# Kernel optimization log

Hardware: AMD Instinct MI355X
Metric: run time of the kernel (lower is better)

Reference implementation:

```python
import jax, jax.numpy as jnp
import numpy as np

B, T, DIM = 8, 2048, 512
DM, EXPAND, NSTATE, HDIM, L = 128, 2, 16, 64, 2
DINNER = DM * EXPAND            # 256
NH = DINNER // HDIM             # 4 heads
CONVDIM = DINNER + 2 * NSTATE   # 288 (n_groups=1)
PROJ = DINNER + CONVDIM + NH    # 548
K = 4                           # conv kernel (HF default)
EPS = 1e-5


def setup_inputs() -> dict:
    key = jax.random.key(0)
    ks = jax.random.split(key, 8)
    s = 0.02
    return {
        "x": jax.random.normal(ks[0], (B, T, DIM), jnp.float32),
        "in_w": jax.random.normal(ks[1], (DIM, DM), jnp.float32) * s,
        "in_b": jnp.zeros((DM,), jnp.float32),
        "norm_w": jnp.ones((L, DM), jnp.float32),
        "inproj_w": jax.random.normal(ks[2], (L, DM, PROJ), jnp.float32) * s,
        "conv_w": jax.random.normal(ks[3], (L, CONVDIM, 1, K), jnp.float32) * 0.2,
        "conv_b": jnp.zeros((L, CONVDIM), jnp.float32),
        "A_log": jnp.log(jax.random.uniform(ks[4], (L, NH), jnp.float32, 1.0, 8.0)),
        "D": jnp.ones((L, NH), jnp.float32),
        "dt_bias": jnp.log(jnp.expm1(jax.random.uniform(ks[5], (L, NH), jnp.float32, 1e-3, 0.1))),
        "gnorm_w": jnp.ones((L, DINNER), jnp.float32),
        "outproj_w": jax.random.normal(ks[6], (L, DINNER, DM), jnp.float32) * s,
        "normf_w": jnp.ones((DM,), jnp.float32),
        "out_w": jax.random.normal(ks[7], (DM, DIM), jnp.float32) * s,
        "out_b": jnp.zeros((DIM,), jnp.float32),
    }


def _rmsnorm(x, w):
    var = jnp.mean(x * x, axis=-1, keepdims=True)
    return x * jax.lax.rsqrt(var + EPS) * w


def _gated_rmsnorm(y, gate, w):
    y = y * jax.nn.silu(gate)
    var = jnp.mean(y * y, axis=-1, keepdims=True)
    return y * jax.lax.rsqrt(var + EPS) * w


def _causal_conv(h, w, b):
    # h: [B,T,C] depthwise causal conv, kernel K, left pad K-1
    out = jax.lax.conv_general_dilated(
        h.swapaxes(1, 2), w, (1,), [(K - 1, 0)],
        feature_group_count=CONVDIM,
        dimension_numbers=("NCH", "OIH", "NCH"))
    return out.swapaxes(1, 2) + b


def _ssd(xs, dt, A, Bm, Cm, Dh):
    # selective state-space scan (math-equivalent to HF Mamba2 chunked SSD)
    # xs [B,T,H,P], dt [B,T,H], A [H], Bm/Cm [B,T,N], Dh [H]
    dA = jnp.exp(dt * A)  # [B,T,H]

    def step(state, inp):
        dA_t, dt_t, x_t, B_t, C_t = inp
        dBx = dt_t[:, :, None, None] * x_t[..., None] * B_t[:, None, None, :]
        state = state * dA_t[:, :, None, None] + dBx  # [B,H,P,N]
        y = jnp.einsum("bhpn,bn->bhp", state, C_t)
        return state, y

    init = jnp.zeros((xs.shape[0], NH, HDIM, NSTATE), xs.dtype)
    _, ys = jax.lax.scan(step, init, (dA.swapaxes(0, 1), dt.swapaxes(0, 1),
                                      xs.swapaxes(0, 1), Bm.swapaxes(0, 1), Cm.swapaxes(0, 1)))
    return ys.swapaxes(0, 1) + xs * Dh[None, None, :, None]


def reference(x, in_w, in_b, norm_w, inproj_w, conv_w, conv_b, A_log, D,
              dt_bias, gnorm_w, outproj_w, normf_w, out_w, out_b):
    h = x @ in_w + in_b  # [B,T,DM]
    for l in range(L):
        res = h
        hn = _rmsnorm(h, norm_w[l])
        proj = hn @ inproj_w[l]  # [B,T,PROJ]
        gate = proj[..., :DINNER]
        hBC = proj[..., DINNER:DINNER + CONVDIM]
        dt = proj[..., DINNER + CONVDIM:]
        hBC = jax.nn.silu(_causal_conv(hBC, conv_w[l], conv_b[l]))
        xs = hBC[..., :DINNER].reshape(B, T, NH, HDIM)
        Bm = hBC[..., DINNER:DINNER + NSTATE]
        Cm = hBC[..., DINNER + NSTATE:]
        A = -jnp.exp(A_log[l])
        dt = jax.nn.softplus(dt + dt_bias[l])  # time_step_limit=(0,inf): no clamp
        y = _ssd(xs, dt, A, Bm, Cm, D[l]).reshape(B, T, DINNER)
        y = _gated_rmsnorm(y, gate, gnorm_w[l])
        h = res + y @ outproj_w[l]
    h = _rmsnorm(h, normf_w)
    pooled = h.mean(axis=1)  # mean pool over T
    return pooled @ out_w + out_b
```

## Files before the change

kernel.cpp:

```cpp
#include <hip/hip_runtime.h>
#include <math.h>

typedef unsigned short ushort_t;
typedef unsigned int uint_t;

#define B_      8
#define T_      2048
#define DIMX    512
#define DM      128
#define DINNER  256
#define NSTATE  16
#define HDIM    64
#define NH      4
#define CONVDIM 288
#define PROJ    548
#define KCONV   4
#define LLAYERS 2
#define QCH     128
#define NC      (T_/QCH)
#define EPSF    1e-5f
#define MTOK    (B_*T_)

#define OFF_H      0u
#define OFF_Z      20119552u
#define OFF_DEC    21168128u
#define OFF_PART   21168640u
#define OFF_WTIN   23396864u
#define OFF_WTINP  23429632u
#define OFF_WTOUT  23503360u
#define OFF_PROJB  23600000u
#define OFF_DTRAW  28100000u
#define OFF_YB     30600000u

__device__ __forceinline__ ushort_t f2b(float f) {
    uint_t u = __builtin_bit_cast(uint_t, f);
    return (ushort_t)((u + 0x7FFFu + ((u >> 16) & 1u)) >> 16);
}
__device__ __forceinline__ float b2f(ushort_t b) {
    uint_t u = ((uint_t)b) << 16;
    return __builtin_bit_cast(float, u);
}
__device__ __forceinline__ float blo(uint_t u) { return b2f((ushort_t)(u & 0xffffu)); }
__device__ __forceinline__ float bhi(uint_t u) { return b2f((ushort_t)(u >> 16)); }

typedef short bf8 __attribute__((ext_vector_type(8)));
typedef float f4v __attribute__((ext_vector_type(4)));

__global__ __launch_bounds__(256) void k_wt_all(
    const float* __restrict__ in_w, const float* __restrict__ inproj_w,
    const float* __restrict__ outproj_w,
    ushort_t* __restrict__ wt_in, ushort_t* __restrict__ wt_inp,
    ushort_t* __restrict__ wt_out)
{
    __shared__ float tile[64][65];
    int idx = blockIdx.x;
    const float* W; ushort_t* Wt; int K, N, k0, n0;
    if (idx < 16) {
        W = in_w; Wt = wt_in; K = 512; N = 128;
        k0 = (idx & 7) * 64; n0 = (idx >> 3) * 64;
    } else if (idx < 52) {
        int r = idx - 16; int l = r / 18; r -= l * 18;
        W = inproj_w + l * 128 * PROJ; Wt = wt_inp + l * 576 * 128; K = 128; N = PROJ;
        k0 = (r & 1) * 64; n0 = (r >> 1) * 64;
    } else {
        int r = idx - 52; int l = r / 8; r -= l * 8;
        W = outproj_w + l * 256 * 128; Wt = wt_out + l * 128 * 256; K = 256; N = 128;
        k0 = (r & 3) * 64; n0 = (r >> 2) * 64;
    }
    const int tid = threadIdx.x;
#pragma unroll
    for (int it = 0; it < 16; ++it) {
        const int e = it * 256 + tid;
        const int kk = e >> 6, nn = e & 63;
        tile[kk][nn] = (n0 + nn < N) ? W[(k0 + kk) * N + (n0 + nn)] : 0.f;
    }
    __syncthreads();
#pragma unroll
    for (int it = 0; it < 16; ++it) {
        const int e = it * 256 + tid;
        const int nn = e >> 6, kk = e & 63;
        Wt[(n0 + nn) * K + k0 + kk] = f2b(tile[kk][nn]);
    }
}

__global__ __launch_bounds__(256) void k_gemm_in(
    const float* __restrict__ x, const ushort_t* __restrict__ Bt,
    const float* __restrict__ ib, float* __restrict__ C)
{
    __shared__ ushort_t Als[64 * 136];
    __shared__ ushort_t Bls[64 * 136];
    const int m0 = blockIdx.x * 64;
    const int tid = threadIdx.x;
    const int lane = tid & 63, w = tid >> 6;
    const int wm = (w >> 1) * 32, wn = (w & 1) * 32;
    const int r16 = lane & 15, q8 = (lane >> 4) * 8;

    f4v acc[2][2][2];
#pragma unroll
    for (int hf = 0; hf < 2; ++hf)
#pragma unroll
        for (int i = 0; i < 2; ++i)
#pragma unroll
            for (int j = 0; j < 2; ++j) acc[hf][i][j] = (f4v)0.f;

    for (int kc = 0; kc < 512; kc += 128) {
#pragma unroll
        for (int i = 0; i < 4; ++i) {
            const int e = i * 2048 + tid * 8;
            const int r = e >> 7, c = e & 127;
            const float4 f0 = *(const float4*)&x[(m0 + r) * 512 + kc + c];
            const float4 f1 = *(const float4*)&x[(m0 + r) * 512 + kc + c + 4];
            uint4 pk;
            pk.x = (uint_t)f2b(f0.x) | ((uint_t)f2b(f0.y) << 16);
            pk.y = (uint_t)f2b(f0.z) | ((uint_t)f2b(f0.w) << 16);
            pk.z = (uint_t)f2b(f1.x) | ((uint_t)f2b(f1.y) << 16);
            pk.w = (uint_t)f2b(f1.z) | ((uint_t)f2b(f1.w) << 16);
            *(uint4*)&Als[r * 136 + c] = pk;
        }
#pragma unroll
        for (int hf = 0; hf < 2; ++hf) {
            const int n0 = hf * 64;
#pragma unroll
            for (int i = 0; i < 4; ++i) {
                const int e = i * 2048 + tid * 8;
                const int r = e >> 7, c = e & 127;
                *(uint4*)&Bls[r * 136 + c] = *(const uint4*)&Bt[(n0 + r) * 512 + kc + c];
            }
            __syncthreads();
#pragma unroll
            for (int kk = 0; kk < 128; kk += 32) {
                const bf8 a0 = *(const bf8*)&Als[(wm + r16) * 136 + kk + q8];
                const bf8 a1 = *(const bf8*)&Als[(wm + 16 + r16) * 136 + kk + q8];
                const bf8 b0 = *(const bf8*)&Bls[(wn + r16) * 136 + kk + q8];
                const bf8 b1 = *(const bf8*)&Bls[(wn + 16 + r16) * 136 + kk + q8];
                acc[hf][0][0] = __builtin_amdgcn_mfma_f32_16x16x32_bf16(a0, b0, acc[hf][0][0], 0, 0, 0);
                acc[hf][0][1] = __builtin_amdgcn_mfma_f32_16x16x32_bf16(a0, b1, acc[hf][0][1], 0, 0, 0);
                acc[hf][1][0] = __builtin_amdgcn_mfma_f32_16x16x32_bf16(a1, b0, acc[hf][1][0], 0, 0, 0);
                acc[hf][1][1] = __builtin_amdgcn_mfma_f32_16x16x32_bf16(a1, b1, acc[hf][1][1], 0, 0, 0);
            }
            __syncthreads();
        }
    }
    const int q4 = (lane >> 4) * 4;
#pragma unroll
    for (int hf = 0; hf < 2; ++hf)
#pragma unroll
        for (int i = 0; i < 2; ++i)
#pragma unroll
            for (int j = 0; j < 2; ++j)
#pragma unroll
                for (int r = 0; r < 4; ++r) {
                    const int grow = m0 + wm + i * 16 + q4 + r;
                    const int gcol = hf * 64 + wn + j * 16 + r16;
                    C[grow * 128 + gcol] = acc[hf][i][j][r] + ib[gcol];
                }
}

__global__ __launch_bounds__(256) void k_gemm_rms(
    const float* __restrict__ h, const float* __restrict__ nw,
    const ushort_t* __restrict__ Bt, ushort_t* __restrict__ projb,
    float* __restrict__ dtraw)
{
    __shared__ ushort_t Als[64 * 136];
    __shared__ ushort_t Bls[64 * 136];
    const int m0 = blockIdx.x * 64;
    const int tid = threadIdx.x;
    const int lane = tid & 63, w = tid >> 6;
    const int wm = (w >> 1) * 32, wn = (w & 1) * 32;
    const int r16 = lane & 15, q8 = (lane >> 4) * 8;
    const int q4 = (lane >> 4) * 4;

#pragma unroll
    for (int i = 0; i < 4; ++i) {
        const int e = i * 2048 + tid * 8;
        const int r = e >> 7, c = e & 127;
        const float4 f0 = *(const float4*)&h[(m0 + r) * 128 + c];
        const float4 f1 = *(const float4*)&h[(m0 + r) * 128 + c + 4];
        float ss = f0.x * f0.x + f0.y * f0.y + f0.z * f0.z + f0.w * f0.w
                 + f1.x * f1.x + f1.y * f1.y + f1.z * f1.z + f1.w * f1.w;
#pragma unroll
        for (int off = 1; off < 16; off <<= 1) ss += __shfl_xor(ss, off);
        const float rs = rsqrtf(ss * (1.f / 128.f) + EPSF);
        const float4 w0 = *(const float4*)&nw[c];
        const float4 w1 = *(const float4*)&nw[c + 4];
        uint4 pk;
        pk.x = (uint_t)f2b(f0.x * rs * w0.x) | ((uint_t)f2b(f0.y * rs * w0.y) << 16);
        pk.y = (uint_t)f2b(f0.z * rs * w0.z) | ((uint_t)f2b(f0.w * rs * w0.w) << 16);
        pk.z = (uint_t)f2b(f1.x * rs * w1.x) | ((uint_t)f2b(f1.y * rs * w1.y) << 16);
        pk.w = (uint_t)f2b(f1.z * rs * w1.z) | ((uint_t)f2b(f1.w * rs * w1.w) << 16);
        *(uint4*)&Als[r * 136 + c] = pk;
    }

#pragma unroll
    for (int half = 0; half < 2; ++half) {
        const int n0 = blockIdx.y * 128 + half * 64;
        if (n0 >= 576) break;
#pragma unroll
        for (int i = 0; i < 4; ++i) {
            const int e = i * 2048 + tid * 8;
            const int r = e >> 7, c = e & 127;
            *(uint4*)&Bls[r * 136 + c] = *(const uint4*)&Bt[(n0 + r) * 128 + c];
        }
        __syncthreads();

        f4v acc[2][2];
#pragma unroll
        for (int i = 0; i < 2; ++i)
#pragma unroll
            for (int j = 0; j < 2; ++j) acc[i][j] = (f4v)0.f;
#pragma unroll
        for (int kk = 0; kk < 128; kk += 32) {
            const bf8 a0 = *(const bf8*)&Als[(wm + r16) * 136 + kk + q8];
            const bf8 a1 = *(const bf8*)&Als[(wm + 16 + r16) * 136 + kk + q8];
            const bf8 b0 = *(const bf8*)&Bls[(wn + r16) * 136 + kk + q8];
            const bf8 b1 = *(const bf8*)&Bls[(wn + 16 + r16) * 136 + kk + q8];
            acc[0][0] = __builtin_amdgcn_mfma_f32_16x16x32_bf16(a0, b0, acc[0][0], 0, 0, 0);
            acc[0][1] = __builtin_amdgcn_mfma_f32_16x16x32_bf16(a0, b1, acc[0][1], 0, 0, 0);
            acc[1][0] = __builtin_amdgcn_mfma_f32_16x16x32_bf16(a1, b0, acc[1][0], 0, 0, 0);
            acc[1][1] = __builtin_amdgcn_mfma_f32_16x16x32_bf16(a1, b1, acc[1][1], 0, 0, 0);
        }
        __syncthreads();

#pragma unroll
        for (int i = 0; i < 2; ++i)
#pragma unroll
            for (int j = 0; j < 2; ++j)
#pragma unroll
                for (int r = 0; r < 4; ++r) {
                    const int grow = m0 + wm + i * 16 + q4 + r;
                    const int gcol = n0 + wn + j * 16 + r16;
                    if (gcol < 544) projb[grow * 544 + gcol] = f2b(acc[i][j][r]);
                    else if (gcol < PROJ) dtraw[grow * 4 + (gcol - 544)] = acc[i][j][r];
                }
    }
}

__global__ __launch_bounds__(256) void k_gemm_gn(
    const ushort_t* __restrict__ yb, const ushort_t* __restrict__ projb,
    const float* __restrict__ gw, const ushort_t* __restrict__ Bt,
    float* __restrict__ C)
{
    __shared__ ushort_t Als[64 * 264];
    __shared__ ushort_t Bls[64 * 136];
    const int m0 = blockIdx.x * 64;
    const int tid = threadIdx.x;
    const int lane = tid & 63, w = tid >> 6;
    const int wm = (w >> 1) * 32, wn = (w & 1) * 32;
    const int r16 = lane & 15, q8 = (lane >> 4) * 8;
    const int q4 = (lane >> 4) * 4;

#pragma unroll
    for (int i = 0; i < 8; ++i) {
        const int e = i * 2048 + tid * 8;
        const int r = e >> 8, c = e & 255;
        const uint4 yv = *(const uint4*)&yb[(m0 + r) * 256 + c];
        const uint4 gv = *(const uint4*)&projb[(m0 + r) * 544 + c];
        const float g0 = blo(gv.x), g1 = bhi(gv.x), g2 = blo(gv.y), g3 = bhi(gv.y);
        const float g4 = blo(gv.z), g5 = bhi(gv.z), g6 = blo(gv.w), g7 = bhi(gv.w);
        float v0 = blo(yv.x) * (g0 / (1.f + __expf(-g0)));
        float v1 = bhi(yv.x) * (g1 / (1.f + __expf(-g1)));
        float v2 = blo(yv.y) * (g2 / (1.f + __expf(-g2)));
        float v3 = bhi(yv.y) * (g3 / (1.f + __expf(-g3)));
        float v4 = blo(yv.z) * (g4 / (1.f + __expf(-g4)));
        float v5 = bhi(yv.z) * (g5 / (1.f + __expf(-g5)));
        float v6 = blo(yv.w) * (g6 / (1.f + __expf(-g6)));
        float v7 = bhi(yv.w) * (g7 / (1.f + __expf(-g7)));
        float ss = v0 * v0 + v1 * v1 + v2 * v2 + v3 * v3
                 + v4 * v4 + v5 * v5 + v6 * v6 + v7 * v7;
#pragma unroll
        for (int off = 1; off < 32; off <<= 1) ss += __shfl_xor(ss, off);
        const float rs = rsqrtf(ss * (1.f / 256.f) + EPSF);
        const float4 w0 = *(const float4*)&gw[c];
        const float4 w1 = *(const float4*)&gw[c + 4];
        uint4 pk;
        pk.x = (uint_t)f2b(v0 * rs * w0.x) | ((uint_t)f2b(v1 * rs * w0.y) << 16);
        pk.y = (uint_t)f2b(v2 * rs * w0.z) | ((uint_t)f2b(v3 * rs * w0.w) << 16);
        pk.z = (uint_t)f2b(v4 * rs * w1.x) | ((uint_t)f2b(v5 * rs * w1.y) << 16);
        pk.w = (uint_t)f2b(v6 * rs * w1.z) | ((uint_t)f2b(v7 * rs * w1.w) << 16);
        *(uint4*)&Als[r * 264 + c] = pk;
    }

#pragma unroll
    for (int half = 0; half < 2; ++half) {
        const int n0 = half * 64;
        f4v acc[2][2];
#pragma unroll
        for (int i = 0; i < 2; ++i)
#pragma unroll
            for (int j = 0; j < 2; ++j) acc[i][j] = (f4v)0.f;

        for (int kc = 0; kc < 256; kc += 128) {
#pragma unroll
            for (int i = 0; i < 4; ++i) {
                const int e = i * 2048 + tid * 8;
                const int r = e >> 7, c = e & 127;
                *(uint4*)&Bls[r * 136 + c] = *(const uint4*)&Bt[(n0 + r) * 256 + kc + c];
            }
            __syncthreads();
#pragma unroll
            for (int kk = 0; kk < 128; kk += 32) {
                const bf8 a0 = *(const bf8*)&Als[(wm + r16) * 264 + kc + kk + q8];
                const bf8 a1 = *(const bf8*)&Als[(wm + 16 + r16) * 264 + kc + kk + q8];
                const bf8 b0 = *(const bf8*)&Bls[(wn + r16) * 136 + kk + q8];
                const bf8 b1 = *(const bf8*)&Bls[(wn + 16 + r16) * 136 + kk + q8];
                acc[0][0] = __builtin_amdgcn_mfma_f32_16x16x32_bf16(a0, b0, acc[0][0], 0, 0, 0);
                acc[0][1] = __builtin_amdgcn_mfma_f32_16x16x32_bf16(a0, b1, acc[0][1], 0, 0, 0);
                acc[1][0] = __builtin_amdgcn_mfma_f32_16x16x32_bf16(a1, b0, acc[1][0], 0, 0, 0);
                acc[1][1] = __builtin_amdgcn_mfma_f32_16x16x32_bf16(a1, b1, acc[1][1], 0, 0, 0);
            }
            __syncthreads();
        }

#pragma unroll
        for (int i = 0; i < 2; ++i)
#pragma unroll
            for (int j = 0; j < 2; ++j)
#pragma unroll
                for (int r = 0; r < 4; ++r) {
                    const int grow = m0 + wm + i * 16 + q4 + r;
                    const int gcol = n0 + wn + j * 16 + r16;
                    C[grow * 128 + gcol] += acc[i][j][r];
                }
    }
}

__device__ __forceinline__ void dt_scan_wave0(
    const float* __restrict__ dtraw, const float* __restrict__ A_log,
    const float* __restrict__ dt_bias, int l, int hh, int m0, int lane,
    float* __restrict__ cumls, float* __restrict__ dtls)
{
    const float Ah = -expf(A_log[l * NH + hh]);
    const float bias = dt_bias[l * NH + hh];
    const float r0 = dtraw[(m0 + lane) * 4 + hh] + bias;
    const float r1 = dtraw[(m0 + 64 + lane) * 4 + hh] + bias;
    const float dt0 = (r0 > 20.f) ? r0 : log1pf(expf(r0));
    const float dt1 = (r1 > 20.f) ? r1 : log1pf(expf(r1));
    float v0 = dt0 * Ah, v1 = dt1 * Ah;
#pragma unroll
    for (int off = 1; off < 64; off <<= 1) {
        const int src = (lane - off) & 63;
        const float s0 = __shfl(v0, src);
        const float s1 = __shfl(v1, src);
        v0 += (lane >= off) ? s0 : 0.f;
        v1 += (lane >= off) ? s1 : s0;
    }
    v1 += v0;
    cumls[lane] = v0; cumls[64 + lane] = v1;
    dtls[lane]  = dt0; dtls[64 + lane]  = dt1;
}

__global__ __launch_bounds__(256) void k_ssd_state(
    const ushort_t* __restrict__ projb, const float* __restrict__ dtraw,
    const float* __restrict__ cw, const float* __restrict__ cb,
    const float* __restrict__ A_log, const float* __restrict__ dt_bias,
    float* __restrict__ zbuf, float* __restrict__ dec, int l)
{
    __shared__ ushort_t Xt[64 * 136];
    __shared__ ushort_t wB[16 * 136];
    __shared__ ushort_t pX[131 * 64];
    __shared__ ushort_t pB[131 * 16];
    __shared__ float cumls[QCH];
    __shared__ float dtls[QCH];
    const int bid = blockIdx.x;
    const int c = bid & (NC - 1);
    if (c == NC - 1) return;
    const int hh = (bid / NC) & (NH - 1);
    const int b = bid / (NC * NH);
    const int m0 = b * T_ + c * QCH;
    const int tid = threadIdx.x;
    const int lane = tid & 63;

    if (tid < 64) {
        dt_scan_wave0(dtraw, A_log, dt_bias, l, hh, m0, lane, cumls, dtls);
    } else {
        const int t0 = c * QCH;
        for (int e = tid - 64; e < 131 * 8; e += 192) {
            const int ls = e >> 3, j = e & 7;
            const int tb = t0 + ls - 3;
            uint4 v; v.x = 0u; v.y = 0u; v.z = 0u; v.w = 0u;
            if (tb >= 0) v = *(const uint4*)&projb[(b * T_ + tb) * 544 + 256 + hh * 64 + j * 8];
            *(uint4*)&pX[ls * 64 + j * 8] = v;
        }
        for (int e = tid - 64; e < 131 * 2; e += 192) {
            const int ls = e >> 1, j = e & 1;
            const int tb = t0 + ls - 3;
            uint4 v; v.x = 0u; v.y = 0u; v.z = 0u; v.w = 0u;
            if (tb >= 0) v = *(const uint4*)&projb[(b * T_ + tb) * 544 + 512 + j * 8];
            *(uint4*)&pB[ls * 16 + j * 8] = v;
        }
    }
    __syncthreads();
    const float clast = cumls[QCH - 1];

    {
        const int p = tid & 63;
        const int s0 = tid >> 6;
        const float* wp = cw + (l * CONVDIM + hh * 64 + p) * KCONV;
        const float bbv = cb[l * CONVDIM + hh * 64 + p];
#pragma unroll
        for (int pass = 0; pass < 32; ++pass) {
            const int s = pass * 4 + s0;
            float a = bbv;
#pragma unroll
            for (int k = 0; k < KCONV; ++k) a += b2f(pX[(s + k) * 64 + p]) * wp[k];
            Xt[p * 136 + s] = f2b(a / (1.f + __expf(-a)));
        }
    }
    {
        const int n = tid & 15;
        const int s0 = tid >> 4;
        const float* wp = cw + (l * CONVDIM + 256 + n) * KCONV;
        const float bbv = cb[l * CONVDIM + 256 + n];
#pragma unroll
        for (int pass = 0; pass < 8; ++pass) {
            const int s = pass * 16 + s0;
            float a = bbv;
#pragma unroll
            for (int k = 0; k < KCONV; ++k) a += b2f(pB[(s + k) * 16 + n]) * wp[k];
            const ushort_t sb = f2b(a / (1.f + __expf(-a)));
            const float w = __expf(clast - cumls[s]) * dtls[s];
            wB[n * 136 + s] = f2b(w * b2f(sb));
        }
    }
    __syncthreads();

    const int w = tid >> 6;
    const int r16 = lane & 15, q8 = (lane >> 4) * 8, q4 = (lane >> 4) * 4;
    f4v acc = (f4v)0.f;
#pragma unroll
    for (int kc = 0; kc < 128; kc += 32) {
        const bf8 a = *(const bf8*)&Xt[(w * 16 + r16) * 136 + kc + q8];
        const bf8 bb = *(const bf8*)&wB[r16 * 136 + kc + q8];
        acc = __builtin_amdgcn_mfma_f32_16x16x32_bf16(a, bb, acc, 0, 0, 0);
    }
#pragma unroll
    for (int r = 0; r < 4; ++r) {
        const int p = w * 16 + q4 + r;
        zbuf[bid * 1024 + p * 16 + r16] = acc[r];
    }
    if (tid == 0) dec[bid] = __expf(clast);
}

__global__ __launch_bounds__(256) void k_ssd_y(
    const ushort_t* __restrict__ projb, const float* __restrict__ dtraw,
    const float* __restrict__ cw, const float* __restrict__ cb,
    const float* __restrict__ A_log, const float* __restrict__ dt_bias,
    const float* __restrict__ zbuf, const float* __restrict__ dec,
    const float* __restrict__ Dvec, ushort_t* __restrict__ yb, int l)
{
    __shared__ ushort_t Xt[64 * 136];
    __shared__ ushort_t BlsT[128 * 40];
    __shared__ ushort_t ClsT[128 * 40];
    __shared__ ushort_t Gls[128 * 136];
    __shared__ ushort_t Spt[64 * 40];
    __shared__ float cumls[QCH];
    __shared__ float dtls[QCH];
    ushort_t* pX = Gls;
    ushort_t* pB = Gls + 131 * 64;
    ushort_t* pC = Gls + 131 * 64 + 131 * 16;
    const int bid = blockIdx.x;
    const int c = bid & (NC - 1);
    const int hh = (bid / NC) & (NH - 1);
    const int b = bid / (NC * NH);
    const int bh = bid >> 4;
    const int m0 = b * T_ + c * QCH;
    const int tid = threadIdx.x;
    const int lane = tid & 63;

    if (tid < 64) {
        dt_scan_wave0(dtraw, A_log, dt_bias, l, hh, m0, lane, cumls, dtls);
    } else {
        const int t0 = c * QCH;
        for (int e = tid - 64; e < 131 * 8; e += 192) {
            const int ls = e >> 3, j = e & 7;
            const int tb = t0 + ls - 3;
            uint4 v; v.x = 0u; v.y = 0u; v.z = 0u; v.w = 0u;
            if (tb >= 0) v = *(const uint4*)&projb[(b * T_ + tb) * 544 + 256 + hh * 64 + j * 8];
            *(uint4*)&pX[ls * 64 + j * 8] = v;
        }
        for (int e = tid - 64; e < 131 * 2; e += 192) {
            const int ls = e >> 1, j = e & 1;
            const int tb = t0 + ls - 3;
            uint4 v0; v0.x = 0u; v0.y = 0u; v0.z = 0u; v0.w = 0u;
            uint4 v1 = v0;
            if (tb >= 0) {
                v0 = *(const uint4*)&projb[(b * T_ + tb) * 544 + 512 + j * 8];
                v1 = *(const uint4*)&projb[(b * T_ + tb) * 544 + 528 + j * 8];
            }
            *(uint4*)&pB[ls * 16 + j * 8] = v0;
            *(uint4*)&pC[ls * 16 + j * 8] = v1;
        }
    }
    __syncthreads();

    {
        const int p = tid & 63;
        const int s0 = tid >> 6;
        const float* wp = cw + (l * CONVDIM + hh * 64 + p) * KCONV;
        const float bbv = cb[l * CONVDIM + hh * 64 + p];
#pragma unroll
        for (int pass = 0; pass < 32; ++pass) {
            const int s = pass * 4 + s0;
            float a = bbv;
#pragma unroll
            for (int k = 0; k < KCONV; ++k) a += b2f(pX[(s + k) * 64 + p]) * wp[k];
            Xt[p * 136 + s] = f2b(a / (1.f + __expf(-a)));
        }
    }
    {
        const int n = tid & 15;
        const int s0 = tid >> 4;
        const float* wpB = cw + (l * CONVDIM + 256 + n) * KCONV;
        const float bbB = cb[l * CONVDIM + 256 + n];
        const float* wpC = cw + (l * CONVDIM + 272 + n) * KCONV;
        const float bbC = cb[l * CONVDIM + 272 + n];
#pragma unroll
        for (int pass = 0; pass < 8; ++pass) {
            const int s = pass * 16 + s0;
            float aB = bbB, aC = bbC;
#pragma unroll
            for (int k = 0; k < KCONV; ++k) {
                aB += b2f(pB[(s + k) * 16 + n]) * wpB[k];
                aC += b2f(pC[(s + k) * 16 + n]) * wpC[k];
            }
            BlsT[s * 40 + n] = f2b(aB / (1.f + __expf(-aB)));
            ClsT[s * 40 + n] = f2b(aC / (1.f + __expf(-aC)));
            BlsT[s * 40 + 16 + n] = 0;
            ClsT[s * 40 + 16 + n] = 0;
        }
    }
    {
        float4 S; S.x = 0.f; S.y = 0.f; S.z = 0.f; S.w = 0.f;
        for (int cc = 0; cc < c; ++cc) {
            const float d = dec[bh * NC + cc];
            const float4 z = *(const float4*)(zbuf + (bh * NC + cc) * 1024 + tid * 4);
            S.x = S.x * d + z.x; S.y = S.y * d + z.y;
            S.z = S.z * d + z.z; S.w = S.w * d + z.w;
        }
        const int p = tid >> 2, n = (tid & 3) * 4;
        Spt[p * 40 + n]     = f2b(S.x);
        Spt[p * 40 + n + 1] = f2b(S.y);
        Spt[p * 40 + n + 2] = f2b(S.z);
        Spt[p * 40 + n + 3] = f2b(S.w);
        Spt[p * 40 + 16 + n]     = 0;
        Spt[p * 40 + 16 + n + 1] = 0;
        Spt[p * 40 + 16 + n + 2] = 0;
        Spt[p * 40 + 16 + n + 3] = 0;
    }
    __syncthreads();

    const int w = tid >> 6;
    const int wrow = w * 32;
    const int r16 = lane & 15, q8 = (lane >> 4) * 8, q4 = (lane >> 4) * 4;
    const float Dh = Dvec[l * NH + hh];

    bf8 cfr[2];
#pragma unroll
    for (int i = 0; i < 2; ++i)
        cfr[i] = *(const bf8*)&ClsT[(wrow + i * 16 + r16) * 40 + q8];

    float cumt[8], et[8];
#pragma unroll
    for (int i = 0; i < 2; ++i)
#pragma unroll
        for (int r = 0; r < 4; ++r) {
            const int t = wrow + i * 16 + q4 + r;
            cumt[i * 4 + r] = cumls[t];
            et[i * 4 + r] = __expf(cumls[t]);
        }

    f4v acc[2][4];
#pragma unroll
    for (int j = 0; j < 4; ++j) {
        const bf8 sf = *(const bf8*)&Spt[(j * 16 + r16) * 40 + q8];
#pragma unroll
        for (int i = 0; i < 2; ++i) {
            f4v z = (f4v)0.f;
            z = __builtin_amdgcn_mfma_f32_16x16x32_bf16(cfr[i], sf, z, 0, 0, 0);
#pragma unroll
            for (int r = 0; r < 4; ++r) {
                const int t = wrow + i * 16 + q4 + r;
                const int p = j * 16 + r16;
                acc[i][j][r] = z[r] * et[i * 4 + r] + Dh * b2f(Xt[p * 136 + t]);
            }
        }
    }

#pragma unroll
    for (int ts = 0; ts < 8; ++ts) {
        const bf8 bf = *(const bf8*)&BlsT[(ts * 16 + r16) * 40 + q8];
        const int s = ts * 16 + r16;
        const float cs = cumls[s];
        const float ds = dtls[s];
#pragma unroll
        for (int i = 0; i < 2; ++i) {
            f4v g = (f4v)0.f;
            g = __builtin_amdgcn_mfma_f32_16x16x32_bf16(cfr[i], bf, g, 0, 0, 0);
#pragma unroll
            for (int r = 0; r < 4; ++r) {
                const int t = wrow + i * 16 + q4 + r;
                const float val = (s <= t) ? __expf(cumt[i * 4 + r] - cs) * ds * g[r] : 0.f;
                Gls[t * 136 + s] = f2b(val);
            }
        }
    }
    __syncthreads();

#pragma unroll
    for (int kc = 0; kc < 128; kc += 32) {
        bf8 af[2];
#pragma unroll
        for (int i = 0; i < 2; ++i)
            af[i] = *(const bf8*)&Gls[(wrow + i * 16 + r16) * 136 + kc + q8];
#pragma unroll
        for (int j = 0; j < 4; ++j) {
            const bf8 xf = *(const bf8*)&Xt[(j * 16 + r16) * 136 + kc + q8];
#pragma unroll
            for (int i = 0; i < 2; ++i)
                acc[i][j] = __builtin_amdgcn_mfma_f32_16x16x32_bf16(af[i], xf, acc[i][j], 0, 0, 0);
        }
    }

#pragma unroll
    for (int i = 0; i < 2; ++i)
#pragma unroll
        for (int r = 0; r < 4; ++r) {
            const int t = wrow + i * 16 + q4 + r;
#pragma unroll
            for (int j = 0; j < 4; ++j) {
                const int p = j * 16 + r16;
                yb[(m0 + t) * DINNER + hh * 64 + p] = f2b(acc[i][j][r]);
            }
        }
}

__global__ __launch_bounds__(256) void k_finalnorm_pool(
    const float* __restrict__ h, const float* __restrict__ nfw,
    float* __restrict__ part)
{
    __shared__ float ht[2048];
    __shared__ float red[256];
    __shared__ float rstd[16];
    __shared__ float padd[256];
    const int tile = blockIdx.x & 127;
    const int b = blockIdx.x >> 7;
    const int m0 = b * T_ + tile * 16;
    const int tid = threadIdx.x;
    for (int e = tid; e < 2048; e += 256) ht[e] = h[m0 * DM + e];
    __syncthreads();
    {
        const int tg = tid >> 4, j0 = tid & 15;
        float p = 0.f;
#pragma unroll
        for (int k = 0; k < 8; ++k) { const float v = ht[tg * 128 + j0 + 16 * k]; p += v * v; }
        red[tid] = p;
    }
    __syncthreads();
    if (tid < 16) {
        float s = 0.f;
#pragma unroll
        for (int q = 0; q < 16; ++q) s += red[tid * 16 + q];
        rstd[tid] = rsqrtf(s * (1.f / 128.f) + EPSF);
    }
    __syncthreads();
    const int d = tid & 127, half = tid >> 7;
    float ps = 0.f;
#pragma unroll
    for (int i0 = 0; i0 < 8; ++i0) { const int i = half + 2 * i0; ps += ht[i * 128 + d] * rstd[i]; }
    padd[tid] = ps;
    __syncthreads();
    if (tid < 128) part[(b * 128 + tile) * 128 + tid] = (padd[tid] + padd[128 + tid]) * nfw[tid];
}

__global__ __launch_bounds__(256) void k_head(
    const float* __restrict__ part, const float* __restrict__ ow,
    const float* __restrict__ ob, float* __restrict__ out)
{
    __shared__ float pooled[128];
    const int b = blockIdx.x;
    const int tid = threadIdx.x;
    if (tid < 128) {
        float s = 0.f;
        for (int tile = 0; tile < 128; ++tile) s += part[(b * 128 + tile) * 128 + tid];
        pooled[tid] = s * (1.f / (float)T_);
    }
    __syncthreads();
    for (int o = tid; o < DIMX; o += 256) {
        float acc = ob[o];
#pragma unroll 4
        for (int d = 0; d < 128; ++d) acc += pooled[d] * ow[d * DIMX + o];
        out[b * DIMX + o] = acc;
    }
}

extern "C" void kernel_launch(void* const* d_in, const int* in_sizes, int n_in,
                              void* d_out, int out_size, void* d_ws, size_t ws_size,
                              hipStream_t stream)
{
    const float* x         = (const float*)d_in[0];
    const float* in_w      = (const float*)d_in[1];
    const float* in_b      = (const float*)d_in[2];
    const float* norm_w    = (const float*)d_in[3];
    const float* inproj_w  = (const float*)d_in[4];
    const float* conv_w    = (const float*)d_in[5];
    const float* conv_b    = (const float*)d_in[6];
    const float* A_log     = (const float*)d_in[7];
    const float* Dvec      = (const float*)d_in[8];
    const float* dt_bias   = (const float*)d_in[9];
    const float* gnorm_w   = (const float*)d_in[10];
    const float* outproj_w = (const float*)d_in[11];
    const float* normf_w   = (const float*)d_in[12];
    const float* out_w     = (const float*)d_in[13];
    const float* out_b     = (const float*)d_in[14];

    float* ws    = (float*)d_ws;
    float* h     = ws + OFF_H;
    float* zbuf  = ws + OFF_Z;
    float* dec   = ws + OFF_DEC;
    float* part  = ws + OFF_PART;
    float* dtraw = ws + OFF_DTRAW;
    ushort_t* projb = (ushort_t*)(ws + OFF_PROJB);
    ushort_t* yb    = (ushort_t*)(ws + OFF_YB);
    ushort_t* wt_in  = (ushort_t*)(ws + OFF_WTIN);
    ushort_t* wt_inp = (ushort_t*)(ws + OFF_WTINP);
    ushort_t* wt_out = (ushort_t*)(ws + OFF_WTOUT);

    k_wt_all<<<68, 256, 0, stream>>>(in_w, inproj_w, outproj_w, wt_in, wt_inp, wt_out);

    k_gemm_in<<<MTOK / 64, 256, 0, stream>>>(x, wt_in, in_b, h);

    for (int l = 0; l < LLAYERS; ++l) {
        k_gemm_rms<<<dim3(MTOK / 64, 5), 256, 0, stream>>>(
            h, norm_w + l * DM, wt_inp + l * 576 * 128, projb, dtraw);
        k_ssd_state<<<B_ * NH * NC, 256, 0, stream>>>(
            projb, dtraw, conv_w, conv_b, A_log, dt_bias, zbuf, dec, l);
        k_ssd_y<<<B_ * NH * NC, 256, 0, stream>>>(
            projb, dtraw, conv_w, conv_b, A_log, dt_bias, zbuf, dec, Dvec, yb, l);
        k_gemm_gn<<<MTOK / 64, 256, 0, stream>>>(
            yb, projb, gnorm_w + l * DINNER, wt_out + l * 128 * 256, h);
    }

    k_finalnorm_pool<<<B_ * (T_ / 16), 256, 0, stream>>>(h, normf_w, part);
    k_head<<<B_, 256, 0, stream>>>(part, out_w, out_b, (float*)d_out);
}
```

Measured before the change: 246.4 us.

## Fuse RMSNorm into preceding GEMM epilogues and fold final norm-pool into last out-proj

The input-projection and out-projection GEMMs now stage their fp32 result tile in shared memory and apply the next layer's RMSNorm there. They write a bf16 normalized activation buffer, so the in-proj GEMM loads bf16 directly instead of re-reading fp32 h and normalizing. The last layer's out-proj instead computes the final RMSNorm and per-block pooled partial sums, which removes the separate final norm-pool kernel and its write of h. This cuts global traffic on h and one launch. In exchange the GEMM epilogues get longer and use more shared memory, and there is an extra bf16 buffer.

```diff
diff --git a/kernel.cpp b/kernel.cpp
--- a/kernel.cpp
+++ b/kernel.cpp
@@ -22,6 +22,7 @@
 #define MTOK    (B_*T_)
 
 #define OFF_H      0u
+#define OFF_HNB    4000000u
 #define OFF_Z      20119552u
 #define OFF_DEC    21168128u
 #define OFF_PART   21168640u
@@ -85,15 +86,19 @@
 
 __global__ __launch_bounds__(256) void k_gemm_in(
     const float* __restrict__ x, const ushort_t* __restrict__ Bt,
-    const float* __restrict__ ib, float* __restrict__ C)
-{
-    __shared__ ushort_t Als[64 * 136];
-    __shared__ ushort_t Bls[64 * 136];
+    const float* __restrict__ ib, const float* __restrict__ nw,
+    float* __restrict__ C, ushort_t* __restrict__ hnb)
+{
+    __shared__ ushort_t sm[64 * 136 * 2];
+    ushort_t* Als = sm;
+    ushort_t* Bls = sm + 64 * 136;
+    float* hls = (float*)sm;
     const int m0 = blockIdx.x * 64;
     const int tid = threadIdx.x;
     const int lane = tid & 63, w = tid >> 6;
     const int wm = (w >> 1) * 32, wn = (w & 1) * 32;
     const int r16 = lane & 15, q8 = (lane >> 4) * 8;
+    const int q4 = (lane >> 4) * 4;
 
     f4v acc[2][2][2];
 #pragma unroll
@@ -141,7 +146,6 @@
             __syncthreads();
         }
     }
-    const int q4 = (lane >> 4) * 4;
 #pragma unroll
     for (int hf = 0; hf < 2; ++hf)
 #pragma unroll
@@ -150,32 +154,19 @@
             for (int j = 0; j < 2; ++j)
 #pragma unroll
                 for (int r = 0; r < 4; ++r) {
-                    const int grow = m0 + wm + i * 16 + q4 + r;
+                    const int lr = wm + i * 16 + q4 + r;
                     const int gcol = hf * 64 + wn + j * 16 + r16;
-                    C[grow * 128 + gcol] = acc[hf][i][j][r] + ib[gcol];
+                    const float v = acc[hf][i][j][r] + ib[gcol];
+                    C[(m0 + lr) * 128 + gcol] = v;
+                    hls[lr * 136 + gcol] = v;
                 }
-}
-
-__global__ __launch_bounds__(256) void k_gemm_rms(
-    const float* __restrict__ h, const float* __restrict__ nw,
-    const ushort_t* __restrict__ Bt, ushort_t* __restrict__ projb,
-    float* __restrict__ dtraw)
-{
-    __shared__ ushort_t Als[64 * 136];
-    __shared__ ushort_t Bls[64 * 136];
-    const int m0 = blockIdx.x * 64;
-    const int tid = threadIdx.x;
-    const int lane = tid & 63, w = tid >> 6;
-    const int wm = (w >> 1) * 32, wn = (w & 1) * 32;
-    const int r16 = lane & 15, q8 = (lane >> 4) * 8;
-    const int q4 = (lane >> 4) * 4;
-
+    __syncthreads();
 #pragma unroll
     for (int i = 0; i < 4; ++i) {
         const int e = i * 2048 + tid * 8;
         const int r = e >> 7, c = e & 127;
-        const float4 f0 = *(const float4*)&h[(m0 + r) * 128 + c];
-        const float4 f1 = *(const float4*)&h[(m0 + r) * 128 + c + 4];
+        const float4 f0 = *(const float4*)&hls[r * 136 + c];
+        const float4 f1 = *(const float4*)&hls[r * 136 + c + 4];
         float ss = f0.x * f0.x + f0.y * f0.y + f0.z * f0.z + f0.w * f0.w
                  + f1.x * f1.x + f1.y * f1.y + f1.z * f1.z + f1.w * f1.w;
 #pragma unroll
@@ -188,7 +179,29 @@
         pk.y = (uint_t)f2b(f0.z * rs * w0.z) | ((uint_t)f2b(f0.w * rs * w0.w) << 16);
         pk.z = (uint_t)f2b(f1.x * rs * w1.x) | ((uint_t)f2b(f1.y * rs * w1.y) << 16);
         pk.w = (uint_t)f2b(f1.z * rs * w1.z) | ((uint_t)f2b(f1.w * rs * w1.w) << 16);
-        *(uint4*)&Als[r * 136 + c] = pk;
+        *(uint4*)&hnb[(m0 + r) * 128 + c] = pk;
+    }
+}
+
+__global__ __launch_bounds__(256) void k_gemm_rms(
+    const ushort_t* __restrict__ hnb,
+    const ushort_t* __restrict__ Bt, ushort_t* __restrict__ projb,
+    float* __restrict__ dtraw)
+{
+    __shared__ ushort_t Als[64 * 136];
+    __shared__ ushort_t Bls[64 * 136];
+    const int m0 = blockIdx.x * 64;
+    const int tid = threadIdx.x;
+    const int lane = tid & 63, w = tid >> 6;
+    const int wm = (w >> 1) * 32, wn = (w & 1) * 32;
+    const int r16 = lane & 15, q8 = (lane >> 4) * 8;
+    const int q4 = (lane >> 4) * 4;
+
+#pragma unroll
+    for (int i = 0; i < 4; ++i) {
+        const int e = i * 2048 + tid * 8;
+        const int r = e >> 7, c = e & 127;
+        *(uint4*)&Als[r * 136 + c] = *(const uint4*)&hnb[(m0 + r) * 128 + c];
     }
 
 #pragma unroll
@@ -235,13 +248,19 @@
     }
 }
 
+template<int MODE>
 __global__ __launch_bounds__(256) void k_gemm_gn(
     const ushort_t* __restrict__ yb, const ushort_t* __restrict__ projb,
     const float* __restrict__ gw, const ushort_t* __restrict__ Bt,
-    float* __restrict__ C)
-{
-    __shared__ ushort_t Als[64 * 264];
-    __shared__ ushort_t Bls[64 * 136];
+    float* __restrict__ C, const float* __restrict__ nw2,
+    ushort_t* __restrict__ hnb, float* __restrict__ part)
+{
+    __shared__ ushort_t sm[64 * 264 + 64 * 136];
+    __shared__ float rstd[64];
+    __shared__ float padd[256];
+    ushort_t* Als = sm;
+    ushort_t* Bls = sm + 64 * 264;
+    float* hls = (float*)sm;
     const int m0 = blockIdx.x * 64;
     const int tid = threadIdx.x;
     const int lane = tid & 63, w = tid >> 6;
@@ -280,15 +299,17 @@
         *(uint4*)&Als[r * 264 + c] = pk;
     }
 
-#pragma unroll
-    for (int half = 0; half < 2; ++half) {
-        const int n0 = half * 64;
-        f4v acc[2][2];
+    f4v acc[2][2][2];
+#pragma unroll
+    for (int hf = 0; hf < 2; ++hf)
 #pragma unroll
         for (int i = 0; i < 2; ++i)
 #pragma unroll
-            for (int j = 0; j < 2; ++j) acc[i][j] = (f4v)0.f;
-
+            for (int j = 0; j < 2; ++j) acc[hf][i][j] = (f4v)0.f;
+
+#pragma unroll
+    for (int hf = 0; hf < 2; ++hf) {
+        const int n0 = hf * 64;
         for (int kc = 0; kc < 256; kc += 128) {
 #pragma unroll
             for (int i = 0; i < 4; ++i) {
@@ -303,24 +324,76 @@
                 const bf8 a1 = *(const bf8*)&Als[(wm + 16 + r16) * 264 + kc + kk + q8];
                 const bf8 b0 = *(const bf8*)&Bls[(wn + r16) * 136 + kk + q8];
                 const bf8 b1 = *(const bf8*)&Bls[(wn + 16 + r16) * 136 + kk + q8];
-                acc[0][0] = __builtin_amdgcn_mfma_f32_16x16x32_bf16(a0, b0, acc[0][0], 0, 0, 0);
-                acc[0][1] = __builtin_amdgcn_mfma_f32_16x16x32_bf16(a0, b1, acc[0][1], 0, 0, 0);
-                acc[1][0] = __builtin_amdgcn_mfma_f32_16x16x32_bf16(a1, b0, acc[1][0], 0, 0, 0);
-                acc[1][1] = __builtin_amdgcn_mfma_f32_16x16x32_bf16(a1, b1, acc[1][1], 0, 0, 0);
+                acc[hf][0][0] = __builtin_amdgcn_mfma_f32_16x16x32_bf16(a0, b0, acc[hf][0][0], 0, 0, 0);
+                acc[hf][0][1] = __builtin_amdgcn_mfma_f32_16x16x32_bf16(a0, b1, acc[hf][0][1], 0, 0, 0);
+                acc[hf][1][0] = __builtin_amdgcn_mfma_f32_16x16x32_bf16(a1, b0, acc[hf][1][0], 0, 0, 0);
+                acc[hf][1][1] = __builtin_amdgcn_mfma_f32_16x16x32_bf16(a1, b1, acc[hf][1][1], 0, 0, 0);
             }
             __syncthreads();
         }
-
+    }
+
+#pragma unroll
+    for (int hf = 0; hf < 2; ++hf)
 #pragma unroll
         for (int i = 0; i < 2; ++i)
 #pragma unroll
             for (int j = 0; j < 2; ++j)
 #pragma unroll
                 for (int r = 0; r < 4; ++r) {
-                    const int grow = m0 + wm + i * 16 + q4 + r;
-                    const int gcol = n0 + wn + j * 16 + r16;
-                    C[grow * 128 + gcol] += acc[i][j][r];
+                    const int lr = wm + i * 16 + q4 + r;
+                    const int gcol = hf * 64 + wn + j * 16 + r16;
+                    const float v = acc[hf][i][j][r] + C[(m0 + lr) * 128 + gcol];
+                    if (MODE == 0) C[(m0 + lr) * 128 + gcol] = v;
+                    hls[lr * 136 + gcol] = v;
                 }
+    __syncthreads();
+
+    if (MODE == 0) {
+#pragma unroll
+        for (int i = 0; i < 4; ++i) {
+            const int e = i * 2048 + tid * 8;
+            const int r = e >> 7, c = e & 127;
+            const float4 f0 = *(const float4*)&hls[r * 136 + c];
+            const float4 f1 = *(const float4*)&hls[r * 136 + c + 4];
+            float ss = f0.x * f0.x + f0.y * f0.y + f0.z * f0.z + f0.w * f0.w
+                     + f1.x * f1.x + f1.y * f1.y + f1.z * f1.z + f1.w * f1.w;
+#pragma unroll
+            for (int off = 1; off < 16; off <<= 1) ss += __shfl_xor(ss, off);
+            const float rs = rsqrtf(ss * (1.f / 128.f) + EPSF);
+            const float4 w0 = *(const float4*)&nw2[c];
+            const float4 w1 = *(const float4*)&nw2[c + 4];
+            uint4 pk;
+            pk.x = (uint_t)f2b(f0.x * rs * w0.x) | ((uint_t)f2b(f0.y * rs * w0.y) << 16);
+            pk.y = (uint_t)f2b(f0.z * rs * w0.z) | ((uint_t)f2b(f0.w * rs * w0.w) << 16);
+            pk.z = (uint_t)f2b(f1.x * rs * w1.x) | ((uint_t)f2b(f1.y * rs * w1.y) << 16);
+            pk.w = (uint_t)f2b(f1.z * rs * w1.z) | ((uint_t)f2b(f1.w * rs * w1.w) << 16);
+            *(uint4*)&hnb[(m0 + r) * 128 + c] = pk;
+        }
+    } else {
+#pragma unroll
+        for (int i = 0; i < 4; ++i) {
+            const int e = i * 2048 + tid * 8;
+            const int r = e >> 7, c = e & 127;
+            const float4 f0 = *(const float4*)&hls[r * 136 + c];
+            const float4 f1 = *(const float4*)&hls[r * 136 + c + 4];
+            float ss = f0.x * f0.x + f0.y * f0.y + f0.z * f0.z + f0.w * f0.w
+                     + f1.x * f1.x + f1.y * f1.y + f1.z * f1.z + f1.w * f1.w;
+#pragma unroll
+            for (int off = 1; off < 16; off <<= 1) ss += __shfl_xor(ss, off);
+            if ((tid & 15) == 0) rstd[r] = rsqrtf(ss * (1.f / 128.f) + EPSF);
+        }
+        __syncthreads();
+        const int d = tid & 127, hv = tid >> 7;
+        float ps = 0.f;
+#pragma unroll
+        for (int i0 = 0; i0 < 32; ++i0) {
+            const int rr = hv + 2 * i0;
+            ps += hls[rr * 136 + d] * rstd[rr];
+        }
+        padd[tid] = ps;
+        __syncthreads();
+        if (tid < 128) part[blockIdx.x * 128 + tid] = (padd[tid] + padd[128 + tid]) * nw2[tid];
     }
 }
 
@@ -634,44 +707,6 @@
         }
 }
 
-__global__ __launch_bounds__(256) void k_finalnorm_pool(
-    const float* __restrict__ h, const float* __restrict__ nfw,
-    float* __restrict__ part)
-{
-    __shared__ float ht[2048];
-    __shared__ float red[256];
-    __shared__ float rstd[16];
-    __shared__ float padd[256];
-    const int tile = blockIdx.x & 127;
-    const int b = blockIdx.x >> 7;
-    const int m0 = b * T_ + tile * 16;
-    const int tid = threadIdx.x;
-    for (int e = tid; e < 2048; e += 256) ht[e] = h[m0 * DM + e];
-    __syncthreads();
-    {
-        const int tg = tid >> 4, j0 = tid & 15;
-        float p = 0.f;
-#pragma unroll
-        for (int k = 0; k < 8; ++k) { const float v = ht[tg * 128 + j0 + 16 * k]; p += v * v; }
-        red[tid] = p;
-    }
-    __syncthreads();
-    if (tid < 16) {
-        float s = 0.f;
-#pragma unroll
-        for (int q = 0; q < 16; ++q) s += red[tid * 16 + q];
-        rstd[tid] = rsqrtf(s * (1.f / 128.f) + EPSF);
-    }
-    __syncthreads();
-    const int d = tid & 127, half = tid >> 7;
-    float ps = 0.f;
-#pragma unroll
-    for (int i0 = 0; i0 < 8; ++i0) { const int i = half + 2 * i0; ps += ht[i * 128 + d] * rstd[i]; }
-    padd[tid] = ps;
-    __syncthreads();
-    if (tid < 128) part[(b * 128 + tile) * 128 + tid] = (padd[tid] + padd[128 + tid]) * nfw[tid];
-}
-
 __global__ __launch_bounds__(256) void k_head(
     const float* __restrict__ part, const float* __restrict__ ow,
     const float* __restrict__ ob, float* __restrict__ out)
@@ -681,7 +716,7 @@
     const int tid = threadIdx.x;
     if (tid < 128) {
         float s = 0.f;
-        for (int tile = 0; tile < 128; ++tile) s += part[(b * 128 + tile) * 128 + tid];
+        for (int tile = 0; tile < 32; ++tile) s += part[(b * 32 + tile) * 128 + tid];
         pooled[tid] = s * (1.f / (float)T_);
     }
     __syncthreads();
@@ -719,6 +754,7 @@
     float* dec   = ws + OFF_DEC;
     float* part  = ws + OFF_PART;
     float* dtraw = ws + OFF_DTRAW;
+    ushort_t* hnb   = (ushort_t*)(ws + OFF_HNB);
     ushort_t* projb = (ushort_t*)(ws + OFF_PROJB);
     ushort_t* yb    = (ushort_t*)(ws + OFF_YB);
     ushort_t* wt_in  = (ushort_t*)(ws + OFF_WTIN);
@@ -727,19 +763,25 @@
 
     k_wt_all<<<68, 256, 0, stream>>>(in_w, inproj_w, outproj_w, wt_in, wt_inp, wt_out);
 
-    k_gemm_in<<<MTOK / 64, 256, 0, stream>>>(x, wt_in, in_b, h);
+    k_gemm_in<<<MTOK / 64, 256, 0, stream>>>(x, wt_in, in_b, norm_w, h, hnb);
 
     for (int l = 0; l < LLAYERS; ++l) {
         k_gemm_rms<<<dim3(MTOK / 64, 5), 256, 0, stream>>>(
-            h, norm_w + l * DM, wt_inp + l * 576 * 128, projb, dtraw);
+            hnb, wt_inp + l * 576 * 128, projb, dtraw);
         k_ssd_state<<<B_ * NH * NC, 256, 0, stream>>>(
             projb, dtraw, conv_w, conv_b, A_log, dt_bias, zbuf, dec, l);
         k_ssd_y<<<B_ * NH * NC, 256, 0, stream>>>(
             projb, dtraw, conv_w, conv_b, A_log, dt_bias, zbuf, dec, Dvec, yb, l);
-        k_gemm_gn<<<MTOK / 64, 256, 0, stream>>>(
-            yb, projb, gnorm_w + l * DINNER, wt_out + l * 128 * 256, h);
-    }
-
-    k_finalnorm_pool<<<B_ * (T_ / 16), 256, 0, stream>>>(h, normf_w, part);
+        if (l == 0) {
+            k_gemm_gn<0><<<MTOK / 64, 256, 0, stream>>>(
+                yb, projb, gnorm_w + l * DINNER, wt_out + l * 128 * 256, h,
+                norm_w + 1 * DM, hnb, nullptr);
+        } else {
+            k_gemm_gn<1><<<MTOK / 64, 256, 0, stream>>>(
+                yb, projb, gnorm_w + l * DINNER, wt_out + l * 128 * 256, h,
+                normf_w, nullptr, part);
+        }
+    }
+
     k_head<<<B_, 256, 0, stream>>>(part, out_w, out_b, (float*)d_out);
 }
```

Measured after the change: 345.8 us. +40.3%, slower.
